# Performance work log

Measured on AMD Instinct MI355X. Metric: run time of the kernel, lower is better.

## Reference

```python
import jax, jax.numpy as jnp
import numpy as np

B, L, C = 8, 256, 64
NEG = -1e30  # large negative instead of -inf to keep grads NaN-free


def setup_inputs() -> dict:
    key = jax.random.key(0)
    k1, k2 = jax.random.split(key)
    scores = jax.random.normal(k1, (B, L, L, C), dtype=jnp.float32)
    lens = jax.random.randint(k2, (B,), 64, L, dtype=jnp.int32)  # sentence lengths in [64, L-1]
    return {"scores": scores, "lens": lens}


def _inside_max(scores, lens):
    """Max-semiring CKY inside pass. scores: [B,L,L,C]; returns logZ per batch [B]."""
    t = jnp.transpose(jnp.max(scores, axis=-1), (1, 2, 0))  # [L,L,B] best label per span
    s0 = jnp.zeros((L, L, B), scores.dtype)                 # chart s[i,j] = best score of span (i,j)
    i = jnp.arange(L)
    j = jnp.arange(L)

    def step(s, w):
        e = jnp.clip(i + w, 0, L - 1)                       # span end, [L]
        k = jnp.clip(i[:, None] + j[None, :], 0, L - 1)     # split points, [L,L]
        left = s[i[:, None], k]                             # s[i, i+j], [L,L,B]
        right = s[k, e[:, None]]                            # s[i+j, i+w], [L,L,B]
        valid = (j[None, :] >= 1) & (j[None, :] < w) & ((i + w) < L)[:, None]
        comb = jnp.max(jnp.where(valid[..., None], left + right, NEG), axis=1)  # [L,B]
        s_l = t[i, e]                                       # label-max span score, [L,B]
        diag = jnp.where(w == 1, s_l, comb + s_l)
        row_ok = ((i + w) < L)[:, None]
        upd = jnp.where(row_ok, diag, s[i, e])
        s = s.at[i, e].set(upd)
        return s, None

    s, _ = jax.lax.scan(step, s0, jnp.arange(1, L))
    lens_c = jnp.clip(lens, 1, L - 1)
    return s[0, lens_c, jnp.arange(B)]                      # logZ (best tree score) per sentence


def reference(scores, lens):
    return _inside_max(scores, lens)
```

## Files before the change

### kernel.cpp

```cpp
#include <hip/hip_runtime.h>

#define LVAL 256
#define T    32
#define ST   36
#define SLAB (T * ST)
#define NB   8
#define NEG  (-1e30f)

#define LDS_FENCE() asm volatile("s_waitcnt lgkmcnt(0)" ::: "memory")

__device__ __forceinline__ size_t sidx(int b, int i, int e) {
    return ((size_t)b << 16) + (i << 8) + e;
}

template<int CTRL>
__device__ __forceinline__ float dpp_max(float v) {
#if __has_builtin(__builtin_amdgcn_mov_dpp)
    int o = __builtin_amdgcn_mov_dpp(__builtin_bit_cast(int, v), CTRL, 0xF, 0xF, true);
    return fmaxf(v, __builtin_bit_cast(float, o));
#else
    return fmaxf(v, __shfl_xor(v, CTRL == 0xB1 ? 1 : 2));
#endif
}

__global__ __launch_bounds__(256) void phase1(const float* __restrict__ scores,
                                              float* __restrict__ s) {
    const int i = blockIdx.x, b = blockIdx.y;
    const int sub = threadIdx.x & 15, slot = threadIdx.x >> 4;
    const float* row = scores + ((((size_t)b * LVAL + i) * LVAL) << 6);
    #pragma unroll 4
    for (int m0 = 0; m0 < LVAL; m0 += 16) {
        const int e = m0 + slot;
        if (e > i) {
            float4 v = *((const float4*)(row + ((size_t)e << 6)) + sub);
            float mx = fmaxf(fmaxf(v.x, v.y), fmaxf(v.z, v.w));
            #pragma unroll
            for (int d = 1; d < 16; d <<= 1) mx = fmaxf(mx, __shfl_xor(mx, d));
            if (sub == 0) s[sidx(b, i, e)] = mx;
        }
    }
}

template<int LP>
__device__ __forceinline__ void diag_step(int lane, int l,
                                          float (*cur)[ST], float (*curT)[ST],
                                          const float (*tb)[ST]) {
    const int cells = T - l;
    const int P = 1 << LP;
    const int c = lane >> LP, p = lane & (P - 1);
    const bool guard = c < cells;
    const int li = guard ? c : 0;
    const int le = guard ? c + l : 0;
    constexpr int NF = 8 >> LP;
    const float tv = tb[li][le];
    float acc = NEG;
    #pragma unroll
    for (int m = 0; m < NF; ++m) {
        const int k0 = 4 * (p + m * P);
        float4 cu = *(const float4*)&cur[li][k0];
        float4 ct = *(const float4*)&curT[le][k0];
        acc = fmaxf(acc, fmaxf(fmaxf(cu.x + ct.x, cu.y + ct.y),
                               fmaxf(cu.z + ct.z, cu.w + ct.w)));
    }
    acc = dpp_max<0xB1>(acc);
    if (LP >= 2) acc = dpp_max<0x4E>(acc);
    const float v = acc + tv;
    if (guard && p == 0) cur[li][le] = v;
    if (guard && p == 1) curT[le][li] = v;
}

__global__ __launch_bounds__(64) void round0(float* __restrict__ s) {
    __shared__ __align__(16) float curS[SLAB], curTS[SLAB], tbS[SLAB];
    float (*cur)[ST]  = (float(*)[ST])curS;
    float (*curT)[ST] = (float(*)[ST])curTS;
    float (*tb)[ST]   = (float(*)[ST])tbS;
    const int bi = blockIdx.x & 7, b = blockIdx.x >> 3;
    const int lane = threadIdx.x;
    const int row = lane >> 1, ch = (lane & 1) * 16;
    const float4 negv = make_float4(NEG, NEG, NEG, NEG);
    #pragma unroll
    for (int j = 0; j < 4; ++j) {
        float4 v = *(const float4*)&s[sidx(b, bi * T + row, bi * T + ch + 4 * j)];
        *(float4*)&tb[row][ch + 4 * j]   = v;
        *(float4*)&cur[row][ch + 4 * j]  = negv;
        *(float4*)&curT[row][ch + 4 * j] = negv;
    }
    LDS_FENCE();
    if (lane < T - 1) {
        float v = tb[lane][lane + 1];
        cur[lane][lane + 1] = v;
        curT[lane + 1][lane] = v;
    }
    LDS_FENCE();
    #pragma unroll 1
    for (int l = 2; l < T; ++l) {
        if (T - l <= 16) diag_step<2>(lane, l, cur, curT, tb);
        else             diag_step<1>(lane, l, cur, curT, tb);
        LDS_FENCE();
    }
    #pragma unroll
    for (int j = 0; j < 4; ++j)
        *(float4*)&s[sidx(b, bi * T + row, bi * T + ch + 4 * j)] =
            *(const float4*)&cur[row][ch + 4 * j];
}

template<int LP>
__device__ __forceinline__ void edge_step(int lane, int l, int D,
                                          const float (*Ae)[ST], const float (*BeT)[ST],
                                          float (*cur)[ST], float (*curT)[ST],
                                          const float (*tb)[ST], const float (*pre)[ST]) {
    const int delta = l - (T - 1);
    const int ad = delta < 0 ? -delta : delta;
    const int cells = T - ad;
    const int P = 1 << LP;
    const int c = lane >> LP, p = lane & (P - 1);
    const bool guard = c < cells;
    const int li = guard ? (delta < 0 ? c + ad : c) : 0;
    const int le = guard ? li + delta : 0;
    constexpr int NF = 8 >> LP;
    const float tv = tb[li][le];
    float acc = pre[li][le];
    #pragma unroll
    for (int m = 0; m < NF; ++m) {
        const int k0 = 4 * (p + m * P);
        float4 a  = *(const float4*)&Ae[li][k0];
        float4 ct = *(const float4*)&curT[le][k0];
        float4 cu = *(const float4*)&cur[li][k0];
        float4 bt = *(const float4*)&BeT[le][k0];
        float s0 = fmaxf(fmaxf(a.x + ct.x, a.y + ct.y), fmaxf(a.z + ct.z, a.w + ct.w));
        float s1 = fmaxf(fmaxf(cu.x + bt.x, cu.y + bt.y), fmaxf(cu.z + bt.z, cu.w + bt.w));
        acc = fmaxf(acc, fmaxf(s0, s1));
    }
    acc = dpp_max<0xB1>(acc);
    if (LP >= 2) acc = dpp_max<0x4E>(acc);
    const float v = (D == 1 && l == 0) ? tv : acc + tv;
    if (guard && p == 0) cur[li][le] = v;
    if (guard && p == 1) curT[le][li] = v;
}

__global__ __launch_bounds__(256) void roundD(float* __restrict__ s, int D,
                                              const int* __restrict__ lens,
                                              float* __restrict__ out) {
    __shared__ __align__(16) float smem[14 * SLAB];
    float (*Ae)[ST]   = (float(*)[ST])(smem + 0 * SLAB);
    float (*BeT)[ST]  = (float(*)[ST])(smem + 1 * SLAB);
    float (*cur)[ST]  = (float(*)[ST])(smem + 2 * SLAB);
    float (*curT)[ST] = (float(*)[ST])(smem + 3 * SLAB);
    float (*tb)[ST]   = (float(*)[ST])(smem + 4 * SLAB);
    float (*pre)[ST]  = (float(*)[ST])(smem + 5 * SLAB);
    float* ATb = smem + 6 * SLAB;
    float* BWb = smem + 10 * SLAB;

    const int nbi = NB - D;
    const int b = blockIdx.x / nbi, bi = blockIdx.x % nbi, be = bi + D;
    const int tid = threadIdx.x, wid = tid >> 6, lane = tid & 63;
    const int lr = tid >> 5, lc = tid & 31;
    const int grow = lane >> 1, gc = (lane & 1) * 16;
    const int gly = lane >> 3, glx = lane & 7, r0 = 4 * gly, c0 = 4 * glx;
    const int nw = (D - 1 < 4) ? (D - 1) : 4;
    float (*AT)[ST] = (float(*)[ST])(ATb + wid * SLAB);
    float (*BW)[ST] = (float(*)[ST])(BWb + wid * SLAB);

    float ag[4][4];
    #pragma unroll
    for (int i = 0; i < 4; ++i)
        #pragma unroll
        for (int j = 0; j < 4; ++j) ag[i][j] = NEG;
    for (int K = bi + 1 + wid; K < be; K += 4) {
        #pragma unroll
        for (int j = 0; j < 4; ++j) {
            float4 av = *(const float4*)&s[sidx(b, bi * T + grow, K * T + gc + 4 * j)];
            AT[gc + 4 * j + 0][grow] = av.x;
            AT[gc + 4 * j + 1][grow] = av.y;
            AT[gc + 4 * j + 2][grow] = av.z;
            AT[gc + 4 * j + 3][grow] = av.w;
            float4 bv = *(const float4*)&s[sidx(b, K * T + grow, be * T + gc + 4 * j)];
            *(float4*)&BW[grow][gc + 4 * j] = bv;
        }
        LDS_FENCE();
        #pragma unroll 4
        for (int k = 0; k < T; ++k) {
            float4 a4 = *(const float4*)&AT[k][r0];
            float4 b4 = *(const float4*)&BW[k][c0];
            const float aa[4] = {a4.x, a4.y, a4.z, a4.w};
            const float bb[4] = {b4.x, b4.y, b4.z, b4.w};
            #pragma unroll
            for (int i = 0; i < 4; ++i)
                #pragma unroll
                for (int j = 0; j < 4; ++j)
                    ag[i][j] = fmaxf(ag[i][j], aa[i] + bb[j]);
        }
        LDS_FENCE();
    }
    if (wid < nw) {
        #pragma unroll
        for (int i = 0; i < 4; ++i)
            *(float4*)&AT[r0 + i][c0] = make_float4(ag[i][0], ag[i][1], ag[i][2], ag[i][3]);
    }
    #pragma unroll
    for (int r = 0; r < 4; ++r) {
        const int row = lr + 8 * r;
        float va = s[sidx(b, bi * T + row, bi * T + lc)];
        Ae[row][lc] = (lc > row) ? va : NEG;
        float vb = s[sidx(b, be * T + row, be * T + lc)];
        BeT[lc][row] = (row < lc) ? vb : NEG;
        tb[row][lc] = s[sidx(b, bi * T + row, be * T + lc)];
        cur[row][lc] = NEG;
        curT[row][lc] = NEG;
    }
    __syncthreads();
    #pragma unroll
    for (int r = 0; r < 4; ++r) {
        const int row = lr + 8 * r;
        float v = NEG;
        for (int w2 = 0; w2 < nw; ++w2)
            v = fmaxf(v, ATb[w2 * SLAB + row * ST + lc]);
        pre[row][lc] = v;
    }
    __syncthreads();

    if (wid == 0) {
        #pragma unroll 1
        for (int l = 0; l < 2 * T - 1; ++l) {
            const int ad0 = (l < T - 1) ? (T - 1 - l) : (l - (T - 1));
            if (ad0 >= 16) edge_step<2>(lane, l, D, Ae, BeT, cur, curT, tb, pre);
            else           edge_step<1>(lane, l, D, Ae, BeT, cur, curT, tb, pre);
            LDS_FENCE();
        }
    }
    __syncthreads();
    #pragma unroll
    for (int r = 0; r < 4; ++r)
        s[sidx(b, bi * T + lr + 8 * r, be * T + lc)] = cur[lr + 8 * r][lc];

    if (D == NB - 1 && tid == 0) {
        int len = lens[b];
        len = len < 1 ? 1 : (len > LVAL - 1 ? LVAL - 1 : len);
        out[b] = (len >= (NB - 1) * T) ? cur[0][len - (NB - 1) * T]
                                       : s[sidx(b, 0, len)];
    }
}

extern "C" void kernel_launch(void* const* d_in, const int* in_sizes, int n_in,
                              void* d_out, int out_size, void* d_ws, size_t ws_size,
                              hipStream_t stream) {
    const float* scores = (const float*)d_in[0];
    const int*   lens   = (const int*)d_in[1];
    float*       out    = (float*)d_out;
    float*       s      = (float*)d_ws;

    phase1<<<dim3(LVAL, 8), 256, 0, stream>>>(scores, s);
    round0<<<64, 64, 0, stream>>>(s);
    for (int D = 1; D < NB; ++D)
        roundD<<<(NB - D) * 8, 256, 0, stream>>>(s, D, lens, out);
}
```

Measured before the change: 352.3 us.

## Fuse diagonal rounds into one persistent kernel with per-batch grid barriers

Replaces the round0 kernel and the seven roundD launches with one persistent kernel of 64 blocks. Each block owns one row tile of one batch and moves through the diagonals, synchronising with the other blocks of its batch through an atomic counter and flag barrier in workspace. Finished row tiles stay in LDS so the A operands are not reloaded from global memory, and the next tb and BeT tiles are prefetched. This removes launch and tail overhead, at the cost of spin-wait barriers that rely on all 64 blocks being resident at once and on a bounded timeout.

```diff
diff --git a/kernel.cpp b/kernel.cpp
--- a/kernel.cpp
+++ b/kernel.cpp
@@ -24,7 +24,11 @@
 }
 
 __global__ __launch_bounds__(256) void phase1(const float* __restrict__ scores,
-                                              float* __restrict__ s) {
+                                              float* __restrict__ s,
+                                              int* __restrict__ bar) {
+    if (blockIdx.x == 0 && blockIdx.y == 0) {
+        for (int k = threadIdx.x; k < 2048; k += 256) bar[k] = 0;
+    }
     const int i = blockIdx.x, b = blockIdx.y;
     const int sub = threadIdx.x & 15, slot = threadIdx.x >> 4;
     const float* row = scores + ((((size_t)b * LVAL + i) * LVAL) << 6);
@@ -67,41 +71,6 @@
     const float v = acc + tv;
     if (guard && p == 0) cur[li][le] = v;
     if (guard && p == 1) curT[le][li] = v;
-}
-
-__global__ __launch_bounds__(64) void round0(float* __restrict__ s) {
-    __shared__ __align__(16) float curS[SLAB], curTS[SLAB], tbS[SLAB];
-    float (*cur)[ST]  = (float(*)[ST])curS;
-    float (*curT)[ST] = (float(*)[ST])curTS;
-    float (*tb)[ST]   = (float(*)[ST])tbS;
-    const int bi = blockIdx.x & 7, b = blockIdx.x >> 3;
-    const int lane = threadIdx.x;
-    const int row = lane >> 1, ch = (lane & 1) * 16;
-    const float4 negv = make_float4(NEG, NEG, NEG, NEG);
-    #pragma unroll
-    for (int j = 0; j < 4; ++j) {
-        float4 v = *(const float4*)&s[sidx(b, bi * T + row, bi * T + ch + 4 * j)];
-        *(float4*)&tb[row][ch + 4 * j]   = v;
-        *(float4*)&cur[row][ch + 4 * j]  = negv;
-        *(float4*)&curT[row][ch + 4 * j] = negv;
-    }
-    LDS_FENCE();
-    if (lane < T - 1) {
-        float v = tb[lane][lane + 1];
-        cur[lane][lane + 1] = v;
-        curT[lane + 1][lane] = v;
-    }
-    LDS_FENCE();
-    #pragma unroll 1
-    for (int l = 2; l < T; ++l) {
-        if (T - l <= 16) diag_step<2>(lane, l, cur, curT, tb);
-        else             diag_step<1>(lane, l, cur, curT, tb);
-        LDS_FENCE();
-    }
-    #pragma unroll
-    for (int j = 0; j < 4; ++j)
-        *(float4*)&s[sidx(b, bi * T + row, bi * T + ch + 4 * j)] =
-            *(const float4*)&cur[row][ch + 4 * j];
 }
 
 template<int LP>
@@ -138,106 +107,189 @@
     if (guard && p == 1) curT[le][li] = v;
 }
 
-__global__ __launch_bounds__(256) void roundD(float* __restrict__ s, int D,
-                                              const int* __restrict__ lens,
-                                              float* __restrict__ out) {
+__device__ __forceinline__ void batch_barrier(int* __restrict__ bar, int b,
+                                              int tid, int ep) {
+    __syncthreads();
+    if (tid == 0) {
+        int* cnt  = bar + b * 256;
+        int* flag = bar + b * 256 + 64;
+        __threadfence();
+        int prev = __hip_atomic_fetch_add(cnt, 1, __ATOMIC_ACQ_REL,
+                                          __HIP_MEMORY_SCOPE_AGENT);
+        if (prev == NB - 1) {
+            __hip_atomic_store(cnt, 0, __ATOMIC_RELAXED, __HIP_MEMORY_SCOPE_AGENT);
+            __hip_atomic_store(flag, ep, __ATOMIC_RELEASE, __HIP_MEMORY_SCOPE_AGENT);
+        } else {
+            int guard = 0;
+            while (__hip_atomic_load(flag, __ATOMIC_RELAXED,
+                                     __HIP_MEMORY_SCOPE_AGENT) < ep) {
+                __builtin_amdgcn_s_sleep(2);
+                if (++guard > (1 << 22)) break;
+            }
+        }
+        __threadfence();
+    }
+    __syncthreads();
+}
+
+__global__ __launch_bounds__(256) void dp_fused(float* __restrict__ s,
+                                                const int* __restrict__ lens,
+                                                float* __restrict__ out,
+                                                int* __restrict__ bar) {
     __shared__ __align__(16) float smem[14 * SLAB];
-    float (*Ae)[ST]   = (float(*)[ST])(smem + 0 * SLAB);
-    float (*BeT)[ST]  = (float(*)[ST])(smem + 1 * SLAB);
-    float (*cur)[ST]  = (float(*)[ST])(smem + 2 * SLAB);
-    float (*curT)[ST] = (float(*)[ST])(smem + 3 * SLAB);
-    float (*tb)[ST]   = (float(*)[ST])(smem + 4 * SLAB);
-    float (*pre)[ST]  = (float(*)[ST])(smem + 5 * SLAB);
-    float* ATb = smem + 6 * SLAB;
+    float* ATb = smem;
+    float (*Ae)[ST]  = (float(*)[ST])(smem + 6 * SLAB);
+    float (*tb)[ST]  = (float(*)[ST])(smem + 7 * SLAB);
+    float (*BeT)[ST] = (float(*)[ST])(smem + 8 * SLAB);
+    float (*cur)[ST] = (float(*)[ST])(smem + 9 * SLAB);
     float* BWb = smem + 10 * SLAB;
-
-    const int nbi = NB - D;
-    const int b = blockIdx.x / nbi, bi = blockIdx.x % nbi, be = bi + D;
+    float (*pre)[ST] = (float(*)[ST])BWb;
+
+    const int b  = blockIdx.x & 7;
+    const int bi = blockIdx.x >> 3;
     const int tid = threadIdx.x, wid = tid >> 6, lane = tid & 63;
     const int lr = tid >> 5, lc = tid & 31;
     const int grow = lane >> 1, gc = (lane & 1) * 16;
     const int gly = lane >> 3, glx = lane & 7, r0 = 4 * gly, c0 = 4 * glx;
-    const int nw = (D - 1 < 4) ? (D - 1) : 4;
-    float (*AT)[ST] = (float(*)[ST])(ATb + wid * SLAB);
+    const int trow = tid >> 3, tc4 = (tid & 7) * 4;
     float (*BW)[ST] = (float(*)[ST])(BWb + wid * SLAB);
 
-    float ag[4][4];
-    #pragma unroll
-    for (int i = 0; i < 4; ++i)
-        #pragma unroll
-        for (int j = 0; j < 4; ++j) ag[i][j] = NEG;
-    for (int K = bi + 1 + wid; K < be; K += 4) {
+    if (wid == 0) {
+        float (*curT0)[ST] = (float(*)[ST])(BWb + 1 * SLAB);
+        float (*t0)[ST]    = (float(*)[ST])(BWb + 2 * SLAB);
+        const float4 negv = make_float4(NEG, NEG, NEG, NEG);
         #pragma unroll
         for (int j = 0; j < 4; ++j) {
-            float4 av = *(const float4*)&s[sidx(b, bi * T + grow, K * T + gc + 4 * j)];
-            AT[gc + 4 * j + 0][grow] = av.x;
-            AT[gc + 4 * j + 1][grow] = av.y;
-            AT[gc + 4 * j + 2][grow] = av.z;
-            AT[gc + 4 * j + 3][grow] = av.w;
-            float4 bv = *(const float4*)&s[sidx(b, K * T + grow, be * T + gc + 4 * j)];
-            *(float4*)&BW[grow][gc + 4 * j] = bv;
+            float4 v = *(const float4*)&s[sidx(b, bi * T + grow, bi * T + gc + 4 * j)];
+            *(float4*)&t0[grow][gc + 4 * j]    = v;
+            *(float4*)&Ae[grow][gc + 4 * j]    = negv;
+            *(float4*)&curT0[grow][gc + 4 * j] = negv;
         }
         LDS_FENCE();
-        #pragma unroll 4
-        for (int k = 0; k < T; ++k) {
-            float4 a4 = *(const float4*)&AT[k][r0];
-            float4 b4 = *(const float4*)&BW[k][c0];
-            const float aa[4] = {a4.x, a4.y, a4.z, a4.w};
-            const float bb[4] = {b4.x, b4.y, b4.z, b4.w};
+        if (lane < T - 1) {
+            float v = t0[lane][lane + 1];
+            Ae[lane][lane + 1] = v;
+            curT0[lane + 1][lane] = v;
+        }
+        LDS_FENCE();
+        #pragma unroll 1
+        for (int l = 2; l < T; ++l) {
+            if (T - l <= 16) diag_step<2>(lane, l, Ae, curT0, t0);
+            else             diag_step<1>(lane, l, Ae, curT0, t0);
+            LDS_FENCE();
+        }
+        #pragma unroll
+        for (int j = 0; j < 4; ++j)
+            *(float4*)&s[sidx(b, bi * T + grow, bi * T + gc + 4 * j)] =
+                *(const float4*)&Ae[grow][gc + 4 * j];
+    } else if (bi + 1 < NB) {
+        for (int idx = tid - 64; idx < 256; idx += 192) {
+            const int row = idx >> 3, c4 = (idx & 7) * 4;
+            *(float4*)&tb[row][c4] =
+                *(const float4*)&s[sidx(b, bi * T + row, (bi + 1) * T + c4)];
+        }
+    }
+
+    #pragma unroll 1
+    for (int D = 1; D < NB; ++D) {
+        batch_barrier(bar, b, tid, D);
+        const int be = bi + D;
+        if (be < NB) {
+            if (D == 1) {
+                float4 v = *(const float4*)&s[sidx(b, be * T + trow, be * T + tc4)];
+                BeT[tc4 + 0][trow] = (trow < tc4 + 0) ? v.x : NEG;
+                BeT[tc4 + 1][trow] = (trow < tc4 + 1) ? v.y : NEG;
+                BeT[tc4 + 2][trow] = (trow < tc4 + 2) ? v.z : NEG;
+                BeT[tc4 + 3][trow] = (trow < tc4 + 3) ? v.w : NEG;
+            }
+            const int nw = (D - 1 < 4) ? (D - 1) : 4;
+            float ag[4][4];
             #pragma unroll
             for (int i = 0; i < 4; ++i)
                 #pragma unroll
-                for (int j = 0; j < 4; ++j)
-                    ag[i][j] = fmaxf(ag[i][j], aa[i] + bb[j]);
-        }
-        LDS_FENCE();
-    }
-    if (wid < nw) {
-        #pragma unroll
-        for (int i = 0; i < 4; ++i)
-            *(float4*)&AT[r0 + i][c0] = make_float4(ag[i][0], ag[i][1], ag[i][2], ag[i][3]);
-    }
-    #pragma unroll
-    for (int r = 0; r < 4; ++r) {
-        const int row = lr + 8 * r;
-        float va = s[sidx(b, bi * T + row, bi * T + lc)];
-        Ae[row][lc] = (lc > row) ? va : NEG;
-        float vb = s[sidx(b, be * T + row, be * T + lc)];
-        BeT[lc][row] = (row < lc) ? vb : NEG;
-        tb[row][lc] = s[sidx(b, bi * T + row, be * T + lc)];
-        cur[row][lc] = NEG;
-        curT[row][lc] = NEG;
-    }
-    __syncthreads();
-    #pragma unroll
-    for (int r = 0; r < 4; ++r) {
-        const int row = lr + 8 * r;
-        float v = NEG;
-        for (int w2 = 0; w2 < nw; ++w2)
-            v = fmaxf(v, ATb[w2 * SLAB + row * ST + lc]);
-        pre[row][lc] = v;
-    }
-    __syncthreads();
-
-    if (wid == 0) {
-        #pragma unroll 1
-        for (int l = 0; l < 2 * T - 1; ++l) {
-            const int ad0 = (l < T - 1) ? (T - 1 - l) : (l - (T - 1));
-            if (ad0 >= 16) edge_step<2>(lane, l, D, Ae, BeT, cur, curT, tb, pre);
-            else           edge_step<1>(lane, l, D, Ae, BeT, cur, curT, tb, pre);
-            LDS_FENCE();
-        }
-    }
-    __syncthreads();
-    #pragma unroll
-    for (int r = 0; r < 4; ++r)
-        s[sidx(b, bi * T + lr + 8 * r, be * T + lc)] = cur[lr + 8 * r][lc];
-
-    if (D == NB - 1 && tid == 0) {
+                for (int j = 0; j < 4; ++j) ag[i][j] = NEG;
+            for (int K = bi + 1 + wid; K < be; K += 4) {
+                const float (*AT)[ST] = (const float(*)[ST])(ATb + (K - bi - 1) * SLAB);
+                #pragma unroll
+                for (int j = 0; j < 4; ++j) {
+                    float4 bv = *(const float4*)&s[sidx(b, K * T + grow, be * T + gc + 4 * j)];
+                    *(float4*)&BW[grow][gc + 4 * j] = bv;
+                }
+                LDS_FENCE();
+                #pragma unroll 4
+                for (int k = 0; k < T; ++k) {
+                    float4 a4 = *(const float4*)&AT[k][r0];
+                    float4 b4 = *(const float4*)&BW[k][c0];
+                    const float aa[4] = {a4.x, a4.y, a4.z, a4.w};
+                    const float bb[4] = {b4.x, b4.y, b4.z, b4.w};
+                    #pragma unroll
+                    for (int i = 0; i < 4; ++i)
+                        #pragma unroll
+                        for (int j = 0; j < 4; ++j)
+                            ag[i][j] = fmaxf(ag[i][j], aa[i] + bb[j]);
+                }
+                LDS_FENCE();
+            }
+            if (wid < nw) {
+                #pragma unroll
+                for (int i = 0; i < 4; ++i)
+                    *(float4*)&BW[r0 + i][c0] =
+                        make_float4(ag[i][0], ag[i][1], ag[i][2], ag[i][3]);
+            }
+            __syncthreads();
+            #pragma unroll
+            for (int r = 0; r < 4; ++r) {
+                const int row = lr + 8 * r;
+                float v = NEG;
+                for (int w2 = 0; w2 < nw; ++w2)
+                    v = fmaxf(v, BWb[w2 * SLAB + row * ST + lc]);
+                pre[row][lc] = v;
+            }
+            __syncthreads();
+            float (*curT)[ST] = (D == NB - 1) ? (float(*)[ST])(BWb + 1 * SLAB)
+                                              : (float(*)[ST])(ATb + (D - 1) * SLAB);
+            #pragma unroll
+            for (int r = 0; r < 4; ++r) {
+                const int row = lr + 8 * r;
+                cur[row][lc]  = NEG;
+                curT[row][lc] = NEG;
+            }
+            __syncthreads();
+            if (wid == 0) {
+                #pragma unroll 1
+                for (int l = 0; l < 2 * T - 1; ++l) {
+                    const int ad0 = (l < T - 1) ? (T - 1 - l) : (l - (T - 1));
+                    if (ad0 >= 16) edge_step<2>(lane, l, D, Ae, BeT, cur, curT, tb, pre);
+                    else           edge_step<1>(lane, l, D, Ae, BeT, cur, curT, tb, pre);
+                    LDS_FENCE();
+                }
+            }
+            __syncthreads();
+            #pragma unroll
+            for (int r = 0; r < 4; ++r)
+                s[sidx(b, bi * T + lr + 8 * r, be * T + lc)] = cur[lr + 8 * r][lc];
+            if (be + 1 < NB) {
+                *(float4*)&tb[trow][tc4] =
+                    *(const float4*)&s[sidx(b, bi * T + trow, (be + 1) * T + tc4)];
+                float4 v = *(const float4*)&s[sidx(b, (be + 1) * T + trow,
+                                                   (be + 1) * T + tc4)];
+                BeT[tc4 + 0][trow] = (trow < tc4 + 0) ? v.x : NEG;
+                BeT[tc4 + 1][trow] = (trow < tc4 + 1) ? v.y : NEG;
+                BeT[tc4 + 2][trow] = (trow < tc4 + 2) ? v.z : NEG;
+                BeT[tc4 + 3][trow] = (trow < tc4 + 3) ? v.w : NEG;
+            }
+        }
+    }
+
+    if (bi == 0 && tid == 0) {
         int len = lens[b];
         len = len < 1 ? 1 : (len > LVAL - 1 ? LVAL - 1 : len);
-        out[b] = (len >= (NB - 1) * T) ? cur[0][len - (NB - 1) * T]
-                                       : s[sidx(b, 0, len)];
+        const int K = len >> 5, off = len & 31;
+        float r;
+        if (K == 0)           r = Ae[0][off];
+        else if (K == NB - 1) r = cur[0][off];
+        else                  r = ATb[(K - 1) * SLAB + off * ST];
+        out[b] = r;
     }
 }
 
@@ -248,9 +300,8 @@
     const int*   lens   = (const int*)d_in[1];
     float*       out    = (float*)d_out;
     float*       s      = (float*)d_ws;
-
-    phase1<<<dim3(LVAL, 8), 256, 0, stream>>>(scores, s);
-    round0<<<64, 64, 0, stream>>>(s);
-    for (int D = 1; D < NB; ++D)
-        roundD<<<(NB - D) * 8, 256, 0, stream>>>(s, D, lens, out);
-}
+    int*         bar    = (int*)((char*)d_ws + ((size_t)(8) << 16) * sizeof(float));
+
+    phase1<<<dim3(LVAL, 8), 256, 0, stream>>>(scores, s, bar);
+    dp_fused<<<64, 256, 0, stream>>>(s, lens, out, bar);
+}
```

Measured after the change: 354.6 us. About the same (+0.7%).
